# Performance work log

Measured on AMD Instinct MI355X. Metric: run time of the kernel, lower is better.

## Reference

```python
import jax, jax.numpy as jnp
import numpy as np

SPARSITY = 0.5      # config['pruning_parameters']['sparsity'] (r)
TEMP = 1e-5         # config['pruning_parameters']['temperature']


def setup_inputs() -> dict:
    key = jax.random.key(0)
    # Weight of an 8192x8192 linear layer; scaled like a trained weight.
    weight = jax.random.normal(key, (8192, 8192), dtype=jnp.float32) * 0.02
    return {"weight": weight}


def reference(weight):
    # Unstructured PDP soft mask (get_mask path, is_pretraining=False).
    n = weight.size  # static
    abs_flat = jnp.abs(weight).reshape(-1)
    # ops.top_k(x, size(x)) == full descending sort
    desc = -jnp.sort(-abs_flat)
    lim = min(max(int((1.0 - SPARSITY) * n), 0), n - 2)  # static python int
    Wh = desc[lim]
    Wt = desc[lim + 1]
    t = 0.5 * (Wh + Wt)  # scalar threshold (self.t = ones*0.5 broadcast)
    # concat(t^2, w^2) along trailing axis of size 2, softmax over it.
    logits = jnp.stack(
        [jnp.broadcast_to(t * t, weight.shape), weight * weight], axis=-1
    ) / TEMP  # [8192, 8192, 2]
    mw = jax.nn.softmax(logits, axis=-1)[..., 1]  # soft keep-probability
    return mw * weight
```

## Files before the change

kernel.cpp:

```cpp
#include <hip/hip_runtime.h>
#include <hip/hip_bf16.h>
#include <stdint.h>


constexpr int H1_BINS = 32768;
constexpr unsigned CAND_CAP = 1u << 22;
constexpr int NBLK_COMPACT = 4096;
constexpr int LCAP = 8192;

struct Sel {
    unsigned b0, r0, b1, r1;
    float    tsq;
    unsigned cand_count;
};

__global__ __launch_bounds__(256) void k_shist(const float4* __restrict__ w4,
                                               unsigned* __restrict__ hist,
                                               long long n4) {
    __shared__ unsigned lh[H1_BINS / 2];
    for (int i = threadIdx.x; i < H1_BINS / 2; i += 256) lh[i] = 0u;
    __syncthreads();
    const long long base = (long long)blockIdx.x * (n4 >> 8);
    for (int j = 0; j < 4; j++) {
        long long idx = base + j * 256 + threadIdx.x;
        if (idx < n4) {
            float4 v = w4[idx];
            unsigned b;
            b = __float_as_uint(fabsf(v.x)) >> 16; atomicAdd(&lh[b >> 1], 1u << ((b & 1) * 16));
            b = __float_as_uint(fabsf(v.y)) >> 16; atomicAdd(&lh[b >> 1], 1u << ((b & 1) * 16));
            b = __float_as_uint(fabsf(v.z)) >> 16; atomicAdd(&lh[b >> 1], 1u << ((b & 1) * 16));
            b = __float_as_uint(fabsf(v.w)) >> 16; atomicAdd(&lh[b >> 1], 1u << ((b & 1) * 16));
        }
    }
    __syncthreads();
    for (int i = threadIdx.x; i < H1_BINS / 2; i += 256) {
        unsigned v = lh[i];
        unsigned lo = v & 0xFFFFu, hi = v >> 16;
        if (lo) atomicAdd(&hist[2 * i],     lo);
        if (hi) atomicAdd(&hist[2 * i + 1], hi);
    }
}

__global__ __launch_bounds__(1024) void k_scan1(const unsigned* __restrict__ hist,
                                                Sel* __restrict__ sel,
                                                const unsigned long long* __restrict__ above_arr,
                                                int above_n,
                                                long long k0, long long k1) {
    __shared__ unsigned long long partial[1024];
    __shared__ unsigned long long suffix[1024];
    __shared__ unsigned long long redbuf[1024];
    const int t = threadIdx.x;
    if (above_arr) {
        unsigned long long a = 0;
        for (int i = t; i < above_n; i += 1024) a += above_arr[i];
        redbuf[t] = a;
        __syncthreads();
        for (int s = 512; s > 0; s >>= 1) {
            if (t < s) redbuf[t] += redbuf[t + s];
            __syncthreads();
        }
        k0 -= (long long)redbuf[0];
        k1 -= (long long)redbuf[0];
        __syncthreads();
    }
    const int C = H1_BINS / 1024;
    unsigned long long s = 0;
    for (int j = 0; j < C; j++) s += hist[t * C + j];
    partial[t] = s;
    __syncthreads();
    if (t == 0) {
        unsigned long long acc = 0;
        for (int j = 1023; j >= 0; j--) { suffix[j] = acc; acc += partial[j]; }
    }
    __syncthreads();
    unsigned long long cum = suffix[t];
    for (int j = C - 1; j >= 0; j--) {
        unsigned bin = (unsigned)(t * C + j);
        unsigned cnt = hist[bin];
        if (cnt) {
            if ((unsigned long long)k0 >= cum && (unsigned long long)k0 < cum + cnt) {
                sel->b0 = bin; sel->r0 = (unsigned)((unsigned long long)k0 - cum);
            }
            if ((unsigned long long)k1 >= cum && (unsigned long long)k1 < cum + cnt) {
                sel->b1 = bin; sel->r1 = (unsigned)((unsigned long long)k1 - cum);
            }
            cum += cnt;
        }
    }
}

__global__ __launch_bounds__(256) void k_compact(const float4* __restrict__ w4,
                                                 Sel* sel,
                                                 unsigned* __restrict__ cand,
                                                 unsigned long long* __restrict__ above_arr,
                                                 long long n4) {
    __shared__ unsigned lbuf[LCAP];
    __shared__ unsigned lcnt;
    __shared__ unsigned gbase;
    if (threadIdx.x == 0) lcnt = 0;
    __syncthreads();
    const unsigned BH = sel->b0, BL = sel->b1;
    unsigned my_above = 0;
    const long long stride = (long long)gridDim.x * 256;
    for (long long i = (long long)blockIdx.x * 256 + threadIdx.x; i < n4; i += stride) {
        float4 v = w4[i];
        #pragma unroll
        for (int c = 0; c < 4; c++) {
            float f = (c == 0) ? v.x : (c == 1) ? v.y : (c == 2) ? v.z : v.w;
            unsigned bits = __float_as_uint(fabsf(f));
            unsigned bin = bits >> 16;
            my_above += (bin > BH) ? 1u : 0u;
            if (bin >= BL && bin <= BH) {
                unsigned p = atomicAdd(&lcnt, 1u);
                if (p < LCAP) lbuf[p] = bits;
            }
        }
    }
    #pragma unroll
    for (int off = 32; off > 0; off >>= 1)
        my_above += __shfl_down(my_above, off, 64);
    __shared__ unsigned long long wsum[4];
    const int wid = threadIdx.x >> 6;
    if ((threadIdx.x & 63) == 0) wsum[wid] = my_above;
    __syncthreads();
    if (threadIdx.x == 0) {
        above_arr[blockIdx.x] = wsum[0] + wsum[1] + wsum[2] + wsum[3];
        unsigned cnt = lcnt < LCAP ? lcnt : LCAP;
        gbase = atomicAdd(&sel->cand_count, cnt);
    }
    __syncthreads();
    const unsigned cnt = lcnt < LCAP ? lcnt : LCAP;
    for (unsigned i = threadIdx.x; i < cnt; i += 256) {
        unsigned dst = gbase + i;
        if (dst < CAND_CAP) cand[dst] = lbuf[i];
    }
}

__global__ __launch_bounds__(256) void k_chist(const unsigned* __restrict__ cand,
                                               const Sel* __restrict__ selS,
                                               unsigned* __restrict__ hist) {
    __shared__ unsigned lh[H1_BINS / 2];
    for (int i = threadIdx.x; i < H1_BINS / 2; i += 256) lh[i] = 0u;
    __syncthreads();
    unsigned count = selS->cand_count;
    if (count > CAND_CAP) count = CAND_CAP;
    const unsigned stride = gridDim.x * 256;
    for (unsigned i = blockIdx.x * 256 + threadIdx.x; i < count; i += stride) {
        unsigned b = cand[i] >> 16;
        atomicAdd(&lh[b >> 1], 1u << ((b & 1) * 16));
    }
    __syncthreads();
    for (int i = threadIdx.x; i < H1_BINS / 2; i += 256) {
        unsigned v = lh[i];
        unsigned lo = v & 0xFFFFu, hi = v >> 16;
        if (lo) atomicAdd(&hist[2 * i],     lo);
        if (hi) atomicAdd(&hist[2 * i + 1], hi);
    }
}

__global__ __launch_bounds__(256) void k_chist2(const unsigned* __restrict__ cand,
                                                const Sel* __restrict__ selS,
                                                const Sel* __restrict__ selC,
                                                unsigned* __restrict__ h2a,
                                                unsigned* __restrict__ h2b) {
    const unsigned b0 = selC->b0, b1 = selC->b1;
    unsigned count = selS->cand_count;
    if (count > CAND_CAP) count = CAND_CAP;
    const unsigned stride = gridDim.x * 256;
    for (unsigned i = blockIdx.x * 256 + threadIdx.x; i < count; i += stride) {
        unsigned bits = cand[i];
        unsigned hi = bits >> 16;
        if (hi == b0) atomicAdd(&h2a[bits & 0xFFFFu], 1u);
        else if (hi == b1) atomicAdd(&h2b[bits & 0xFFFFu], 1u);
    }
}

__global__ __launch_bounds__(1024) void k_scan2(const unsigned* __restrict__ h2a,
                                                const unsigned* __restrict__ h2b,
                                                Sel* __restrict__ sel) {
    __shared__ unsigned long long partial[1024];
    __shared__ unsigned long long suffix[1024];
    __shared__ unsigned lowres[2];
    const int t = threadIdx.x;
    const unsigned b0 = sel->b0, b1 = sel->b1;
    const bool same = (b0 == b1);
    const unsigned long long r0 = sel->r0, r1 = sel->r1;
    const int C = 65536 / 1024;
    for (int phase = 0; phase < 2; phase++) {
        const unsigned* __restrict__ h = (phase == 0) ? h2a : h2b;
        if (phase == 1 && same) break;
        unsigned long long s = 0;
        for (int j = 0; j < C; j++) s += h[t * C + j];
        partial[t] = s;
        __syncthreads();
        if (t == 0) {
            unsigned long long acc = 0;
            for (int j = 1023; j >= 0; j--) { suffix[j] = acc; acc += partial[j]; }
        }
        __syncthreads();
        unsigned long long cum = suffix[t];
        for (int j = C - 1; j >= 0; j--) {
            unsigned bin = (unsigned)(t * C + j);
            unsigned cnt = h[bin];
            if (cnt) {
                if (phase == 0) {
                    if (r0 >= cum && r0 < cum + cnt) lowres[0] = bin;
                    if (same && r1 >= cum && r1 < cum + cnt) lowres[1] = bin;
                } else {
                    if (r1 >= cum && r1 < cum + cnt) lowres[1] = bin;
                }
                cum += cnt;
            }
        }
        __syncthreads();
    }
    if (t == 0) {
        float v0 = __uint_as_float((b0 << 16) | lowres[0]);
        float v1 = __uint_as_float((b1 << 16) | lowres[1]);
        float tt = 0.5f * (v0 + v1);
        sel->tsq = tt * tt;
    }
}

__global__ __launch_bounds__(256) void k_mask(const float4* __restrict__ w4,
                                              float4* __restrict__ o4,
                                              const Sel* __restrict__ sel,
                                              long long n4) {
    const float tsq = sel->tsq;
    const long long stride = (long long)gridDim.x * 256;
    for (long long i = (long long)blockIdx.x * 256 + threadIdx.x; i < n4; i += stride) {
        float4 v = w4[i];
        float4 o;
        o.x = v.x / (1.0f + __expf((tsq - v.x * v.x) * 1e5f));
        o.y = v.y / (1.0f + __expf((tsq - v.y * v.y) * 1e5f));
        o.z = v.z / (1.0f + __expf((tsq - v.z * v.z) * 1e5f));
        o.w = v.w / (1.0f + __expf((tsq - v.w * v.w) * 1e5f));
        o4[i] = o;
    }
}

extern "C" void kernel_launch(void* const* d_in, const int* in_sizes, int n_in,
                              void* d_out, int out_size, void* d_ws, size_t ws_size,
                              hipStream_t stream) {
    const float* w = (const float*)d_in[0];
    float* out = (float*)d_out;
    const long long n  = (long long)in_sizes[0];
    const long long n4 = n / 4;

    uint8_t* ws = (uint8_t*)d_ws;
    unsigned*           hist_s    = (unsigned*)ws;
    unsigned*           chist     = (unsigned*)(ws + 131072);
    unsigned*           h2a       = (unsigned*)(ws + 262144);
    unsigned*           h2b       = (unsigned*)(ws + 524288);
    Sel*                selS      = (Sel*)(ws + 786432);
    Sel*                selC      = (Sel*)(ws + 786432 + 64);
    unsigned long long* above_arr = (unsigned long long*)(ws + 786432 + 128);
    unsigned*           cand      = (unsigned*)(ws + 1048576);

    hipMemsetAsync(ws, 0, 786432 + 128 + NBLK_COMPACT * sizeof(unsigned long long), stream);

    long long lim = n / 2;
    if (lim > n - 2) lim = n - 2;
    const long long k0 = lim, k1 = lim + 1;

    const long long m = 256LL * 4096;
    const long long c = 8192;
    const long long rhi = m / 2 - c;
    const long long rlo = m / 2 + c;

    k_shist  <<<256, 256, 0, stream>>>((const float4*)w, hist_s, n4);
    k_scan1  <<<1, 1024, 0, stream>>>(hist_s, selS, nullptr, 0, rhi, rlo);
    k_compact<<<NBLK_COMPACT, 256, 0, stream>>>((const float4*)w, selS, cand, above_arr, n4);
    k_chist  <<<256, 256, 0, stream>>>(cand, selS, chist);
    k_scan1  <<<1, 1024, 0, stream>>>(chist, selC, above_arr, NBLK_COMPACT, k0, k1);
    k_chist2 <<<256, 256, 0, stream>>>(cand, selS, selC, h2a, h2b);
    k_scan2  <<<1, 1024, 0, stream>>>(h2a, h2b, selC);
    k_mask   <<<8192, 256, 0, stream>>>((const float4*)w, (float4*)out, selC, n4);
}
```

Baseline: 664.6 us.

## Fuse radix-select pipeline into one persistent cooperative kernel with grid syncs

```diff
diff --git a/kernel.cpp b/kernel.cpp
--- a/kernel.cpp
+++ b/kernel.cpp
@@ -1,279 +1,264 @@
 #include <hip/hip_runtime.h>
-#include <hip/hip_bf16.h>
+#include <hip/hip_cooperative_groups.h>
 #include <stdint.h>
 
-
-constexpr int H1_BINS = 32768;
+namespace cg = cooperative_groups;
+
+
+typedef float floatx4 __attribute__((ext_vector_type(4)));
+
+constexpr int NB = 1024;
+constexpr int NT = 256;
+constexpr long long GSZ = (long long)NB * NT;
 constexpr unsigned CAND_CAP = 1u << 22;
-constexpr int NBLK_COMPACT = 4096;
 constexpr int LCAP = 8192;
-
-struct Sel {
-    unsigned b0, r0, b1, r1;
-    float    tsq;
-    unsigned cand_count;
-};
-
-__global__ __launch_bounds__(256) void k_shist(const float4* __restrict__ w4,
-                                               unsigned* __restrict__ hist,
-                                               long long n4) {
-    __shared__ unsigned lh[H1_BINS / 2];
-    for (int i = threadIdx.x; i < H1_BINS / 2; i += 256) lh[i] = 0u;
-    __syncthreads();
-    const long long base = (long long)blockIdx.x * (n4 >> 8);
-    for (int j = 0; j < 4; j++) {
-        long long idx = base + j * 256 + threadIdx.x;
+constexpr int BRW = 1024;
+constexpr long long CMARG = 8192;
+
+constexpr long long ZWORDS = 661520 / 4;
+
+__global__ __launch_bounds__(NT, 4) void k_pdp(const float4* __restrict__ w4,
+                                               float4* __restrict__ o4,
+                                               uint8_t* __restrict__ ws,
+                                               long long n4, long long k0, long long k1)
+{
+    unsigned* hist_s = (unsigned*)(ws);
+    unsigned* h2a    = (unsigned*)(ws + 131072);
+    unsigned* h2b    = (unsigned*)(ws + 393216);
+    unsigned* h2ac   = (unsigned*)(ws + 655360);
+    unsigned* h2bc   = (unsigned*)(ws + 656384);
+    unsigned* chistB = (unsigned*)(ws + 657408);
+    unsigned long long* above = (unsigned long long*)(ws + 661504);
+    unsigned* cand_cnt = (unsigned*)(ws + 661512);
+    unsigned* cand   = (unsigned*)(ws + 1048576);
+    unsigned* zbase  = (unsigned*)(ws);
+
+    __shared__ unsigned sh[9224];
+
+    cg::grid_group grid = cg::this_grid();
+    const int tid = threadIdx.x;
+    const int bid = blockIdx.x;
+    const long long gtid = (long long)bid * NT + tid;
+
+    for (long long i = gtid; i < ZWORDS; i += GSZ) zbase[i] = 0u;
+    grid.sync();
+
+    for (int i = tid; i < 8192; i += NT) sh[i] = 0u;
+    __syncthreads();
+    {
+        const long long base4 = (long long)bid * (n4 >> 10);
+        const long long idx = base4 + tid;
         if (idx < n4) {
             float4 v = w4[idx];
-            unsigned b;
-            b = __float_as_uint(fabsf(v.x)) >> 16; atomicAdd(&lh[b >> 1], 1u << ((b & 1) * 16));
-            b = __float_as_uint(fabsf(v.y)) >> 16; atomicAdd(&lh[b >> 1], 1u << ((b & 1) * 16));
-            b = __float_as_uint(fabsf(v.z)) >> 16; atomicAdd(&lh[b >> 1], 1u << ((b & 1) * 16));
-            b = __float_as_uint(fabsf(v.w)) >> 16; atomicAdd(&lh[b >> 1], 1u << ((b & 1) * 16));
-        }
-    }
-    __syncthreads();
-    for (int i = threadIdx.x; i < H1_BINS / 2; i += 256) {
-        unsigned v = lh[i];
-        unsigned lo = v & 0xFFFFu, hi = v >> 16;
-        if (lo) atomicAdd(&hist[2 * i],     lo);
-        if (hi) atomicAdd(&hist[2 * i + 1], hi);
-    }
-}
-
-__global__ __launch_bounds__(1024) void k_scan1(const unsigned* __restrict__ hist,
-                                                Sel* __restrict__ sel,
-                                                const unsigned long long* __restrict__ above_arr,
-                                                int above_n,
-                                                long long k0, long long k1) {
-    __shared__ unsigned long long partial[1024];
-    __shared__ unsigned long long suffix[1024];
-    __shared__ unsigned long long redbuf[1024];
-    const int t = threadIdx.x;
-    if (above_arr) {
-        unsigned long long a = 0;
-        for (int i = t; i < above_n; i += 1024) a += above_arr[i];
-        redbuf[t] = a;
-        __syncthreads();
-        for (int s = 512; s > 0; s >>= 1) {
-            if (t < s) redbuf[t] += redbuf[t + s];
-            __syncthreads();
-        }
-        k0 -= (long long)redbuf[0];
-        k1 -= (long long)redbuf[0];
-        __syncthreads();
-    }
-    const int C = H1_BINS / 1024;
-    unsigned long long s = 0;
-    for (int j = 0; j < C; j++) s += hist[t * C + j];
-    partial[t] = s;
-    __syncthreads();
-    if (t == 0) {
-        unsigned long long acc = 0;
-        for (int j = 1023; j >= 0; j--) { suffix[j] = acc; acc += partial[j]; }
-    }
-    __syncthreads();
-    unsigned long long cum = suffix[t];
-    for (int j = C - 1; j >= 0; j--) {
-        unsigned bin = (unsigned)(t * C + j);
-        unsigned cnt = hist[bin];
-        if (cnt) {
-            if ((unsigned long long)k0 >= cum && (unsigned long long)k0 < cum + cnt) {
-                sel->b0 = bin; sel->r0 = (unsigned)((unsigned long long)k0 - cum);
-            }
-            if ((unsigned long long)k1 >= cum && (unsigned long long)k1 < cum + cnt) {
-                sel->b1 = bin; sel->r1 = (unsigned)((unsigned long long)k1 - cum);
-            }
-            cum += cnt;
-        }
-    }
-}
-
-__global__ __launch_bounds__(256) void k_compact(const float4* __restrict__ w4,
-                                                 Sel* sel,
-                                                 unsigned* __restrict__ cand,
-                                                 unsigned long long* __restrict__ above_arr,
-                                                 long long n4) {
-    __shared__ unsigned lbuf[LCAP];
-    __shared__ unsigned lcnt;
-    __shared__ unsigned gbase;
-    if (threadIdx.x == 0) lcnt = 0;
-    __syncthreads();
-    const unsigned BH = sel->b0, BL = sel->b1;
-    unsigned my_above = 0;
-    const long long stride = (long long)gridDim.x * 256;
-    for (long long i = (long long)blockIdx.x * 256 + threadIdx.x; i < n4; i += stride) {
+            float f[4] = {v.x, v.y, v.z, v.w};
+            #pragma unroll
+            for (int c = 0; c < 4; c++) {
+                unsigned bin = __float_as_uint(fabsf(f[c])) >> 16;
+                if (bin < 16384)
+                    atomicAdd(&sh[bin >> 1], 1u << ((bin & 1) * 16));
+                else
+                    atomicAdd(&hist_s[bin], 1u);
+            }
+        }
+    }
+    __syncthreads();
+    for (int i = tid; i < 8192; i += NT) {
+        unsigned v = sh[i];
+        if (v) {
+            unsigned lo = v & 0xFFFFu, hi = v >> 16;
+            if (lo) atomicAdd(&hist_s[2 * i],     lo);
+            if (hi) atomicAdd(&hist_s[2 * i + 1], hi);
+        }
+    }
+    grid.sync();
+
+    unsigned BH, BL;
+    {
+        const int base = tid * 128;
+        unsigned psum = 0;
+        for (int j = 0; j < 128; j++) psum += hist_s[base + j];
+        sh[tid] = psum;
+        __syncthreads();
+        if (tid == 0) {
+            unsigned acc = 0;
+            for (int t = NT - 1; t >= 0; t--) { sh[256 + t] = acc; acc += sh[t]; }
+            sh[516] = acc;
+        }
+        __syncthreads();
+        const unsigned total = sh[516];
+        long long rhi = (long long)(total / 2) - CMARG; if (rhi < 0) rhi = 0;
+        long long rlo = (long long)(total / 2) + CMARG;
+        if (rlo > (long long)total - 1) rlo = (long long)total - 1;
+        unsigned long long cum = sh[256 + tid];
+        for (int j = 127; j >= 0; j--) {
+            unsigned bin = (unsigned)(base + j);
+            unsigned cnt = hist_s[bin];
+            if (cnt) {
+                if ((unsigned long long)rhi >= cum && (unsigned long long)rhi < cum + cnt) sh[517] = bin;
+                if ((unsigned long long)rlo >= cum && (unsigned long long)rlo < cum + cnt) sh[518] = bin;
+                cum += cnt;
+            }
+        }
+        __syncthreads();
+        BH = sh[517]; BL = sh[518];
+        if (BH - BL >= (unsigned)BRW) BL = BH - (BRW - 1);
+        __syncthreads();
+    }
+
+    {
+        unsigned* lbuf = sh;
+        unsigned* binc = sh + 8192;
+        for (int i = tid; i < 1024; i += NT) binc[i] = 0u;
+        if (tid == 0) sh[9216] = 0u;
+        __syncthreads();
+        unsigned my_above = 0;
+        #pragma unroll 2
+        for (long long i = gtid; i < n4; i += GSZ) {
+            float4 v = w4[i];
+            float f[4] = {v.x, v.y, v.z, v.w};
+            #pragma unroll
+            for (int c = 0; c < 4; c++) {
+                unsigned bits = __float_as_uint(fabsf(f[c]));
+                unsigned bin = bits >> 16;
+                my_above += (bin > BH) ? 1u : 0u;
+                if (bin >= BL && bin <= BH) {
+                    unsigned p = atomicAdd(&sh[9216], 1u);
+                    if (p < (unsigned)LCAP) lbuf[p] = bits;
+                    atomicAdd(&binc[bin - BL], 1u);
+                }
+            }
+        }
+        #pragma unroll
+        for (int off = 32; off > 0; off >>= 1)
+            my_above += __shfl_down(my_above, off, 64);
+        if ((tid & 63) == 0 && my_above)
+            atomicAdd(above, (unsigned long long)my_above);
+        __syncthreads();
+        for (int i = tid; i < 1024; i += NT) {
+            unsigned c0 = binc[i];
+            if (c0) atomicAdd(&chistB[i], c0);
+        }
+        const unsigned lc = sh[9216] < (unsigned)LCAP ? sh[9216] : (unsigned)LCAP;
+        if (tid == 0) sh[9217] = atomicAdd(cand_cnt, lc);
+        __syncthreads();
+        const unsigned gb = sh[9217];
+        for (unsigned i = tid; i < lc; i += NT) {
+            unsigned dst = gb + i;
+            if (dst < CAND_CAP) cand[dst] = lbuf[i];
+        }
+    }
+    grid.sync();
+
+    unsigned b0, r0, b1, r1, candN;
+    if (tid == 0) {
+        unsigned long long A = *above;
+        unsigned long long k0p = (unsigned long long)(k0 - (long long)A);
+        unsigned long long k1p = (unsigned long long)(k1 - (long long)A);
+        unsigned long long cum = 0;
+        unsigned bb0 = BL, rr0 = 0, bb1 = BL, rr1 = 0;
+        for (int b = (int)BH; b >= (int)BL; b--) {
+            unsigned cnt = chistB[b - (int)BL];
+            if (cnt) {
+                if (k0p >= cum && k0p < cum + cnt) { bb0 = (unsigned)b; rr0 = (unsigned)(k0p - cum); }
+                if (k1p >= cum && k1p < cum + cnt) { bb1 = (unsigned)b; rr1 = (unsigned)(k1p - cum); }
+                cum += cnt;
+            }
+        }
+        sh[9218] = bb0; sh[9219] = rr0; sh[9220] = bb1; sh[9221] = rr1;
+        unsigned cc = *cand_cnt;
+        sh[9222] = cc < CAND_CAP ? cc : CAND_CAP;
+    }
+    __syncthreads();
+    b0 = sh[9218]; r0 = sh[9219]; b1 = sh[9220]; r1 = sh[9221]; candN = sh[9222];
+    __syncthreads();
+
+    for (int i = tid; i < 512; i += NT) sh[i] = 0u;
+    __syncthreads();
+    for (long long i = gtid; i < (long long)candN; i += GSZ) {
+        unsigned bits = cand[i];
+        unsigned hi = bits >> 16, lo = bits & 0xFFFFu;
+        if (hi == b0)      { atomicAdd(&h2a[lo], 1u); atomicAdd(&sh[lo >> 8], 1u); }
+        else if (hi == b1) { atomicAdd(&h2b[lo], 1u); atomicAdd(&sh[256 + (lo >> 8)], 1u); }
+    }
+    __syncthreads();
+    {
+        unsigned ca = sh[tid], cb = sh[256 + tid];
+        if (ca) atomicAdd(&h2ac[tid], ca);
+        if (cb) atomicAdd(&h2bc[tid], cb);
+    }
+    grid.sync();
+
+    auto resolve = [&](unsigned rank, const unsigned* fine, const unsigned* coarse) -> unsigned {
+        __syncthreads();
+        sh[tid] = coarse[tid];
+        __syncthreads();
+        if (tid == 0) {
+            unsigned long long cum = 0; unsigned seg = 0, rem = 0;
+            for (int s = 255; s >= 0; s--) {
+                unsigned c0 = sh[s];
+                if (c0) {
+                    if ((unsigned long long)rank >= cum && (unsigned long long)rank < cum + c0) {
+                        seg = (unsigned)s; rem = (unsigned)((unsigned long long)rank - cum);
+                    }
+                    cum += c0;
+                }
+            }
+            sh[512] = seg; sh[513] = rem;
+        }
+        __syncthreads();
+        const unsigned seg = sh[512], rem = sh[513];
+        sh[tid] = fine[seg * 256 + tid];
+        __syncthreads();
+        if (tid == 0) {
+            unsigned long long cum = 0; unsigned binlo = 0;
+            for (int j = 255; j >= 0; j--) {
+                unsigned c0 = sh[j];
+                if (c0) {
+                    if ((unsigned long long)rem >= cum && (unsigned long long)rem < cum + c0) binlo = (unsigned)j;
+                    cum += c0;
+                }
+            }
+            sh[514] = seg * 256 + binlo;
+        }
+        __syncthreads();
+        return sh[514];
+    };
+    const unsigned lo0 = resolve(r0, h2a, h2ac);
+    const unsigned lo1 = (b1 == b0) ? resolve(r1, h2a, h2ac) : resolve(r1, h2b, h2bc);
+    const float v0 = __uint_as_float((b0 << 16) | lo0);
+    const float v1 = __uint_as_float((b1 << 16) | lo1);
+    const float th = 0.5f * (v0 + v1);
+    const float tsq = th * th;
+
+    floatx4* __restrict__ onat = (floatx4*)o4;
+    #pragma unroll 2
+    for (long long i = n4 - 1 - gtid; i >= 0; i -= GSZ) {
         float4 v = w4[i];
-        #pragma unroll
-        for (int c = 0; c < 4; c++) {
-            float f = (c == 0) ? v.x : (c == 1) ? v.y : (c == 2) ? v.z : v.w;
-            unsigned bits = __float_as_uint(fabsf(f));
-            unsigned bin = bits >> 16;
-            my_above += (bin > BH) ? 1u : 0u;
-            if (bin >= BL && bin <= BH) {
-                unsigned p = atomicAdd(&lcnt, 1u);
-                if (p < LCAP) lbuf[p] = bits;
-            }
-        }
-    }
-    #pragma unroll
-    for (int off = 32; off > 0; off >>= 1)
-        my_above += __shfl_down(my_above, off, 64);
-    __shared__ unsigned long long wsum[4];
-    const int wid = threadIdx.x >> 6;
-    if ((threadIdx.x & 63) == 0) wsum[wid] = my_above;
-    __syncthreads();
-    if (threadIdx.x == 0) {
-        above_arr[blockIdx.x] = wsum[0] + wsum[1] + wsum[2] + wsum[3];
-        unsigned cnt = lcnt < LCAP ? lcnt : LCAP;
-        gbase = atomicAdd(&sel->cand_count, cnt);
-    }
-    __syncthreads();
-    const unsigned cnt = lcnt < LCAP ? lcnt : LCAP;
-    for (unsigned i = threadIdx.x; i < cnt; i += 256) {
-        unsigned dst = gbase + i;
-        if (dst < CAND_CAP) cand[dst] = lbuf[i];
-    }
-}
-
-__global__ __launch_bounds__(256) void k_chist(const unsigned* __restrict__ cand,
-                                               const Sel* __restrict__ selS,
-                                               unsigned* __restrict__ hist) {
-    __shared__ unsigned lh[H1_BINS / 2];
-    for (int i = threadIdx.x; i < H1_BINS / 2; i += 256) lh[i] = 0u;
-    __syncthreads();
-    unsigned count = selS->cand_count;
-    if (count > CAND_CAP) count = CAND_CAP;
-    const unsigned stride = gridDim.x * 256;
-    for (unsigned i = blockIdx.x * 256 + threadIdx.x; i < count; i += stride) {
-        unsigned b = cand[i] >> 16;
-        atomicAdd(&lh[b >> 1], 1u << ((b & 1) * 16));
-    }
-    __syncthreads();
-    for (int i = threadIdx.x; i < H1_BINS / 2; i += 256) {
-        unsigned v = lh[i];
-        unsigned lo = v & 0xFFFFu, hi = v >> 16;
-        if (lo) atomicAdd(&hist[2 * i],     lo);
-        if (hi) atomicAdd(&hist[2 * i + 1], hi);
-    }
-}
-
-__global__ __launch_bounds__(256) void k_chist2(const unsigned* __restrict__ cand,
-                                                const Sel* __restrict__ selS,
-                                                const Sel* __restrict__ selC,
-                                                unsigned* __restrict__ h2a,
-                                                unsigned* __restrict__ h2b) {
-    const unsigned b0 = selC->b0, b1 = selC->b1;
-    unsigned count = selS->cand_count;
-    if (count > CAND_CAP) count = CAND_CAP;
-    const unsigned stride = gridDim.x * 256;
-    for (unsigned i = blockIdx.x * 256 + threadIdx.x; i < count; i += stride) {
-        unsigned bits = cand[i];
-        unsigned hi = bits >> 16;
-        if (hi == b0) atomicAdd(&h2a[bits & 0xFFFFu], 1u);
-        else if (hi == b1) atomicAdd(&h2b[bits & 0xFFFFu], 1u);
-    }
-}
-
-__global__ __launch_bounds__(1024) void k_scan2(const unsigned* __restrict__ h2a,
-                                                const unsigned* __restrict__ h2b,
-                                                Sel* __restrict__ sel) {
-    __shared__ unsigned long long partial[1024];
-    __shared__ unsigned long long suffix[1024];
-    __shared__ unsigned lowres[2];
-    const int t = threadIdx.x;
-    const unsigned b0 = sel->b0, b1 = sel->b1;
-    const bool same = (b0 == b1);
-    const unsigned long long r0 = sel->r0, r1 = sel->r1;
-    const int C = 65536 / 1024;
-    for (int phase = 0; phase < 2; phase++) {
-        const unsigned* __restrict__ h = (phase == 0) ? h2a : h2b;
-        if (phase == 1 && same) break;
-        unsigned long long s = 0;
-        for (int j = 0; j < C; j++) s += h[t * C + j];
-        partial[t] = s;
-        __syncthreads();
-        if (t == 0) {
-            unsigned long long acc = 0;
-            for (int j = 1023; j >= 0; j--) { suffix[j] = acc; acc += partial[j]; }
-        }
-        __syncthreads();
-        unsigned long long cum = suffix[t];
-        for (int j = C - 1; j >= 0; j--) {
-            unsigned bin = (unsigned)(t * C + j);
-            unsigned cnt = h[bin];
-            if (cnt) {
-                if (phase == 0) {
-                    if (r0 >= cum && r0 < cum + cnt) lowres[0] = bin;
-                    if (same && r1 >= cum && r1 < cum + cnt) lowres[1] = bin;
-                } else {
-                    if (r1 >= cum && r1 < cum + cnt) lowres[1] = bin;
-                }
-                cum += cnt;
-            }
-        }
-        __syncthreads();
-    }
-    if (t == 0) {
-        float v0 = __uint_as_float((b0 << 16) | lowres[0]);
-        float v1 = __uint_as_float((b1 << 16) | lowres[1]);
-        float tt = 0.5f * (v0 + v1);
-        sel->tsq = tt * tt;
-    }
-}
-
-__global__ __launch_bounds__(256) void k_mask(const float4* __restrict__ w4,
-                                              float4* __restrict__ o4,
-                                              const Sel* __restrict__ sel,
-                                              long long n4) {
-    const float tsq = sel->tsq;
-    const long long stride = (long long)gridDim.x * 256;
-    for (long long i = (long long)blockIdx.x * 256 + threadIdx.x; i < n4; i += stride) {
-        float4 v = w4[i];
-        float4 o;
+        floatx4 o;
         o.x = v.x / (1.0f + __expf((tsq - v.x * v.x) * 1e5f));
         o.y = v.y / (1.0f + __expf((tsq - v.y * v.y) * 1e5f));
         o.z = v.z / (1.0f + __expf((tsq - v.z * v.z) * 1e5f));
         o.w = v.w / (1.0f + __expf((tsq - v.w * v.w) * 1e5f));
-        o4[i] = o;
+        __builtin_nontemporal_store(o, &onat[i]);
     }
 }
 
 extern "C" void kernel_launch(void* const* d_in, const int* in_sizes, int n_in,
                               void* d_out, int out_size, void* d_ws, size_t ws_size,
                               hipStream_t stream) {
-    const float* w = (const float*)d_in[0];
-    float* out = (float*)d_out;
+    const float4* w4 = (const float4*)d_in[0];
+    float4* o4 = (float4*)d_out;
     const long long n  = (long long)in_sizes[0];
-    const long long n4 = n / 4;
-
-    uint8_t* ws = (uint8_t*)d_ws;
-    unsigned*           hist_s    = (unsigned*)ws;
-    unsigned*           chist     = (unsigned*)(ws + 131072);
-    unsigned*           h2a       = (unsigned*)(ws + 262144);
-    unsigned*           h2b       = (unsigned*)(ws + 524288);
-    Sel*                selS      = (Sel*)(ws + 786432);
-    Sel*                selC      = (Sel*)(ws + 786432 + 64);
-    unsigned long long* above_arr = (unsigned long long*)(ws + 786432 + 128);
-    unsigned*           cand      = (unsigned*)(ws + 1048576);
-
-    hipMemsetAsync(ws, 0, 786432 + 128 + NBLK_COMPACT * sizeof(unsigned long long), stream);
+    long long n4 = n / 4;
 
     long long lim = n / 2;
     if (lim > n - 2) lim = n - 2;
-    const long long k0 = lim, k1 = lim + 1;
-
-    const long long m = 256LL * 4096;
-    const long long c = 8192;
-    const long long rhi = m / 2 - c;
-    const long long rlo = m / 2 + c;
-
-    k_shist  <<<256, 256, 0, stream>>>((const float4*)w, hist_s, n4);
-    k_scan1  <<<1, 1024, 0, stream>>>(hist_s, selS, nullptr, 0, rhi, rlo);
-    k_compact<<<NBLK_COMPACT, 256, 0, stream>>>((const float4*)w, selS, cand, above_arr, n4);
-    k_chist  <<<256, 256, 0, stream>>>(cand, selS, chist);
-    k_scan1  <<<1, 1024, 0, stream>>>(chist, selC, above_arr, NBLK_COMPACT, k0, k1);
-    k_chist2 <<<256, 256, 0, stream>>>(cand, selS, selC, h2a, h2b);
-    k_scan2  <<<1, 1024, 0, stream>>>(h2a, h2b, selC);
-    k_mask   <<<8192, 256, 0, stream>>>((const float4*)w, (float4*)out, selC, n4);
+    long long k0 = lim, k1 = lim + 1;
+
+    uint8_t* ws = (uint8_t*)d_ws;
+
+    void* args[] = { (void*)&w4, (void*)&o4, (void*)&ws,
+                     (void*)&n4, (void*)&k0, (void*)&k1 };
+    (void)hipLaunchCooperativeKernel((const void*)k_pdp, dim3(NB), dim3(NT),
+                                     args, 0, stream);
 }
```

After: 1.070 ms. 1.61x slower.
